# Optimization experiments

Measured on AMD Instinct MI355X. Metric: run time of the kernel, lower is better.

Reference implementation:

```python
import jax, jax.numpy as jnp
import numpy as np

B, S, D, H, L, K = 16, 384, 512, 8, 4, 7
HD = D // H
MAXLEN = 400


def _pos_encoding(d=D, max_len=MAXLEN):
    # Faithful to the (unusual) torch loop: even idx i -> sin(pos/10000**(2i/d)),
    # odd idx i+1 -> cos(pos/10000**(2(i+1)/d))
    pe = np.zeros((max_len, d), dtype=np.float32)
    pos = np.arange(max_len, dtype=np.float64)[:, None]
    i = np.arange(0, d, 2)
    pe[:, i] = np.sin(pos / 10000.0 ** (2 * i / d))
    pe[:, i + 1] = np.cos(pos / 10000.0 ** (2 * (i + 1) / d))
    return jnp.asarray(pe)

POS_ENC = _pos_encoding()


def layer_norm(x, g, b, eps=1e-5):
    m = jnp.mean(x, -1, keepdims=True)
    v = jnp.mean((x - m) ** 2, -1, keepdims=True)
    return (x - m) * jax.lax.rsqrt(v + eps) * g + b


def dsconv(x, dw_w, pw_w, pw_b):
    # x: [B,S,D]; depthwise conv1d (no bias) then pointwise 1x1 (bias)
    xc = jnp.transpose(x, (0, 2, 1))  # [B,D,S]
    y = jax.lax.conv_general_dilated(
        xc, dw_w, window_strides=(1,), padding=[(K // 2, K // 2)],
        dimension_numbers=("NCH", "OIH", "NCH"), feature_group_count=D)  # [B,D,S]
    return jnp.einsum("bcs,oc->bso", y, pw_w) + pw_b  # [B,S,D]


def setup_inputs():
    key = jax.random.key(0)
    ks = jax.random.split(key, 16)
    sc = 0.02
    inp = {
        "x": jax.random.normal(ks[0], (B, S, D), jnp.float32),
        "mask": jax.random.randint(ks[1], (B, S), 0, 2, jnp.int32),
        "dw_w": jax.random.normal(ks[2], (L, D, 1, K), jnp.float32) * sc,
        "pw_w": jax.random.normal(ks[3], (L, D, D), jnp.float32) * sc,
        "pw_b": jnp.zeros((L, D), jnp.float32),
        "conv_ln_g": jnp.ones((L, D), jnp.float32),
        "conv_ln_b": jnp.zeros((L, D), jnp.float32),
        "pos_ln_g": jnp.ones((D,), jnp.float32),
        "pos_ln_b": jnp.zeros((D,), jnp.float32),
        "wq": jax.random.normal(ks[4], (D, D), jnp.float32) * sc,
        "bq": jnp.zeros((D,), jnp.float32),
        "wk": jax.random.normal(ks[5], (D, D), jnp.float32) * sc,
        "bk": jnp.zeros((D,), jnp.float32),
        "wv": jax.random.normal(ks[6], (D, D), jnp.float32) * sc,
        "bv": jnp.zeros((D,), jnp.float32),
        "wo": jax.random.normal(ks[7], (D, D), jnp.float32) * sc,
        "bo": jnp.zeros((D,), jnp.float32),
        "ff_ln_g": jnp.ones((D,), jnp.float32),
        "ff_ln_b": jnp.zeros((D,), jnp.float32),
        "ff_w": jax.random.normal(ks[8], (D, D), jnp.float32) * sc,
        "ff_b": jnp.zeros((D,), jnp.float32),
    }
    return inp


def attention(x, mask, wq, bq, wk, bk, wv, bv, wo, bo):
    def heads(w, b):
        y = jnp.einsum("bsd,od->bso", x, w) + b
        return jnp.transpose(y.reshape(B, S, H, HD), (0, 2, 1, 3))  # [B,H,S,HD]
    q, k, v = heads(wq, bq), heads(wk, bk), heads(wv, bv)
    energy = jnp.einsum("bhqd,bhkd->bhqk", q, k) / jnp.sqrt(jnp.float32(HD))
    m = (mask == 1)[:, None, None, :]  # [B,1,1,S]
    energy = jnp.where(m, jnp.float32(-1e10), energy)
    alpha = jax.nn.softmax(energy, axis=-1)  # dropout = identity (eval)
    a = jnp.einsum("bhqk,bhkd->bhqd", alpha, v)
    a = jnp.transpose(a, (0, 2, 1, 3)).reshape(B, S, D)
    return jnp.einsum("bsd,od->bso", a, wo) + bo


def reference(x, mask, dw_w, pw_w, pw_b, conv_ln_g, conv_ln_b, pos_ln_g, pos_ln_b,
              wq, bq, wk, bk, wv, bv, wo, bo, ff_ln_g, ff_ln_b, ff_w, ff_b):
    out = x + POS_ENC[None, :S, :]
    res = out
    out = layer_norm(out, pos_ln_g, pos_ln_b)
    for i in range(L):
        out = jax.nn.relu(dsconv(out, dw_w[i], pw_w[i], pw_b[i]))
        out = out + res  # dropout = identity (eval)
        res = out
        out = layer_norm(out, conv_ln_g[i], conv_ln_b[i])
    out = attention(out, mask, wq, bq, wk, bk, wv, bv, wo, bo)
    out = out + res
    res = out
    out = layer_norm(out, ff_ln_g, ff_ln_b)
    out = jax.nn.relu(jnp.einsum("bsd,od->bso", out, ff_w) + ff_b)
    return out + res
```

## Files before the change

kernel.cpp:

```cpp
#include <hip/hip_runtime.h>

#define BB 16
#define SS 384
#define DD 512
#define HH 8
#define HDIM 64
#define LLAY 4
#define KW 7
#define MM (BB*SS)

typedef unsigned short u16;
typedef unsigned int u32;
typedef short short8v __attribute__((ext_vector_type(8)));
typedef float floatx4 __attribute__((ext_vector_type(4)));

__device__ __forceinline__ float bf2f(u16 u) {
    union { u32 i; float f; } v; v.i = ((u32)u) << 16; return v.f;
}
__device__ __forceinline__ u16 f2bf(float f) {
    union { float f; u32 i; } v; v.f = f;
    return (u16)((v.i + 0x7FFFu + ((v.i >> 16) & 1u)) >> 16);
}
__device__ __forceinline__ bool sniff_f32(const void* dtp) {
    return *((const u32*)dtp) == 0x3F800000u;
}
__device__ __forceinline__ float ldf(const void* p, long i, bool f32) {
    return f32 ? ((const float*)p)[i] : bf2f(((const u16*)p)[i]);
}
__device__ __forceinline__ short8v ldfrag_scalar(const void* p, long i, bool f32) {
    short8v r;
    if (f32) {
        const float* q = (const float*)p + i;
#pragma unroll
        for (int j = 0; j < 8; j++) r[j] = (short)f2bf(q[j]);
    } else {
        r = *(const short8v*)((const u16*)p + i);
    }
    return r;
}

__device__ __forceinline__ void load_lds16(const u16* g, u16* l) {
    __builtin_amdgcn_global_load_lds((const __attribute__((address_space(1))) void*)g,
                                     (__attribute__((address_space(3))) void*)l, 16, 0, 0);
}
__device__ __forceinline__ int swz(int row) { return (row & 3) ^ ((row >> 2) & 3); }
__device__ __forceinline__ short8v lds_frag(const u16* buf, int row, int quad) {
    return *(const short8v*)(buf + ((size_t)row * 4 + (quad ^ swz(row))) * 8);
}

#define WCV_DW 2359296
#define WCV_TOT (WCV_DW + LLAY*KW*DD)
__global__ __launch_bounds__(256) void cvt_weights_kernel(
    const void* __restrict__ pw_w, const void* __restrict__ wq,
    const void* __restrict__ wk, const void* __restrict__ wv,
    const void* __restrict__ wo, const void* __restrict__ ff_w,
    const void* __restrict__ dw_w,
    u16* __restrict__ dst, const void* __restrict__ dtp) {
    const bool f32 = sniff_f32(dtp);
    const int i = blockIdx.x * 256 + threadIdx.x;
    if (i >= WCV_TOT) return;
    const void* src; long idx;
    if (i < 1048576) { src = pw_w; idx = i; }
    else if (i < WCV_DW) {
        const int j = i - 1048576;
        const int m = j >> 18;
        idx = j & 262143;
        src = (m == 0) ? wq : (m == 1) ? wk : (m == 2) ? wv : (m == 3) ? wo : ff_w;
    } else {
        const int j = i - WCV_DW;
        const int l = j / (KW * DD);
        const int r1 = j % (KW * DD);
        const int t = r1 / DD, c = r1 % DD;
        src = dw_w; idx = ((long)l * DD + c) * KW + t;
    }
    dst[i] = f2bf(ldf(src, idx, f32));
}

__global__ __launch_bounds__(256) void posln_kernel(const void* __restrict__ x,
                                                    const void* __restrict__ g,
                                                    const void* __restrict__ bvec,
                                                    u16* __restrict__ res,
                                                    u16* __restrict__ out,
                                                    const void* __restrict__ dtp) {
    const bool f32 = sniff_f32(dtp);
    const int row = blockIdx.x;
    const int s = row % SS;
    const int tid = threadIdx.x;
    float v[2];
#pragma unroll
    for (int i = 0; i < 2; i++) {
        const int d = tid + i * 256;
        const float freq = __expf(-(float)d * 0.035977892078032f);
        const float arg = (float)s * freq;
        const float pe = (d & 1) ? cosf(arg) : sinf(arg);
        v[i] = ldf(x, (long)row * DD + d, f32) + pe;
        res[row * DD + d] = f2bf(v[i]);
    }
    float sum = v[0] + v[1], sq = v[0] * v[0] + v[1] * v[1];
#pragma unroll
    for (int off = 32; off; off >>= 1) { sum += __shfl_down(sum, off); sq += __shfl_down(sq, off); }
    __shared__ float red[4][2];
    const int wv = tid >> 6;
    if ((tid & 63) == 0) { red[wv][0] = sum; red[wv][1] = sq; }
    __syncthreads();
    sum = red[0][0] + red[1][0] + red[2][0] + red[3][0];
    sq  = red[0][1] + red[1][1] + red[2][1] + red[3][1];
    const float mean = sum * (1.f / DD);
    const float rstd = rsqrtf(sq * (1.f / DD) - mean * mean + 1e-5f);
#pragma unroll
    for (int i = 0; i < 2; i++) {
        const int d = tid + i * 256;
        out[row * DD + d] = f2bf((v[i] - mean) * rstd * ldf(g, d, f32) + ldf(bvec, d, f32));
    }
}

template <int VEC>
__global__ __launch_bounds__(256) void dwconv_kernel(const u16* __restrict__ in,
                                                     const void* __restrict__ w, int layer,
                                                     u16* __restrict__ out,
                                                     const void* __restrict__ dtp) {
    if constexpr (VEC) {
        const int bsw = (blockIdx.x & 7) * (MM * DD / 8 / 256 / 8) + (blockIdx.x >> 3);
        const int idx = bsw * 256 + threadIdx.x;
        const int c8 = (idx & 63) * 8;
        const int ms = idx >> 6;
        const int s = ms % SS;
        const u16* wl = (const u16*)w + (size_t)layer * KW * DD;
        float acc[8] = {0, 0, 0, 0, 0, 0, 0, 0};
#pragma unroll
        for (int t = 0; t < KW; t++) {
            const int ss2 = s + t - 3;
            if (ss2 >= 0 && ss2 < SS) {
                const short8v iv = *(const short8v*)(in + (size_t)(ms + t - 3) * DD + c8);
                const short8v wv = *(const short8v*)(wl + t * DD + c8);
#pragma unroll
                for (int j = 0; j < 8; j++)
                    acc[j] += bf2f((u16)iv[j]) * bf2f((u16)wv[j]);
            }
        }
        short8v ov;
#pragma unroll
        for (int j = 0; j < 8; j++) ov[j] = (short)f2bf(acc[j]);
        *(short8v*)(out + (size_t)ms * DD + c8) = ov;
    } else {
        const bool f32 = sniff_f32(dtp);
        const long woff = (long)layer * DD * KW;
        const int idx = blockIdx.x * 256 + threadIdx.x;
        const int c = idx & (DD - 1);
        const int ms = idx >> 9;
        const int s = ms % SS;
        float acc = 0.f;
#pragma unroll
        for (int t = 0; t < KW; t++) {
            const int ss2 = s + t - 3;
            if (ss2 >= 0 && ss2 < SS)
                acc += bf2f(in[(ms + t - 3) * DD + c]) * ldf(w, woff + c * KW + t, f32);
        }
        out[idx] = f2bf(acc);
    }
}

__device__ __forceinline__ void stage_tile(const u16* A, const u16* W, int m0,
                                           u16* Abuf, u16* Wbuf, int tid, int k0) {
#pragma unroll
    for (int j = 0; j < 8; j++) {
        const int c = j * 256 + tid;
        const int row = c >> 2;
        const int kpart = (c & 3) ^ swz(row);
        load_lds16(W + (size_t)row * DD + k0 + kpart * 8, Wbuf + (size_t)c * 8);
    }
    if (tid < 128) {
        const int row = tid >> 2;
        const int kpart = (tid & 3) ^ swz(row);
        load_lds16(A + (size_t)(m0 + row) * DD + k0 + kpart * 8, Abuf + (size_t)tid * 8);
    }
}

__device__ __forceinline__ void kloop_lds(const u16* A, const u16* W, int m0,
                                          u16* Abuf, u16* Wbuf,
                                          int tid, int wave, int ln15, int quad,
                                          floatx4 acc[2][8]) {
    stage_tile(A, W, m0, Abuf, Wbuf, tid, 0);
    __syncthreads();
    for (int ks = 0; ks < 16; ks++) {
        const int cur = ks & 1;
        u16* Ab = Abuf + cur * (32 * 32);
        u16* Wb = Wbuf + cur * (DD * 32);
        if (ks < 15)
            stage_tile(A, W, m0, Abuf + (cur ^ 1) * (32 * 32),
                       Wbuf + (cur ^ 1) * (DD * 32), tid, (ks + 1) * 32);
        const short8v a0 = lds_frag(Ab, ln15, quad);
        const short8v a1 = lds_frag(Ab, 16 + ln15, quad);
#pragma unroll
        for (int nt = 0; nt < 8; nt++) {
            const short8v b = lds_frag(Wb, wave * 128 + nt * 16 + ln15, quad);
            acc[0][nt] = __builtin_amdgcn_mfma_f32_16x16x32_bf16(a0, b, acc[0][nt], 0, 0, 0);
            acc[1][nt] = __builtin_amdgcn_mfma_f32_16x16x32_bf16(a1, b, acc[1][nt], 0, 0, 0);
        }
        __syncthreads();
    }
}

template <int RELU, int DO_LN, int FINAL, int WVEC>
__global__ __launch_bounds__(256, 2) void gemm32_kernel(
    const u16* __restrict__ A, const void* __restrict__ W, int wlayer,
    const void* __restrict__ bias, const void* __restrict__ g,
    const void* __restrict__ bvec, int blayer,
    const u16* __restrict__ res_in, u16* __restrict__ res_out,
    void* __restrict__ out, const void* __restrict__ dtp) {
    const bool f32 = sniff_f32(dtp);
    const long woff = (long)wlayer * DD * DD;
    const long voff = (long)blayer * DD;
    __shared__ float part[4][2][16][2];
    __shared__ __align__(16) u16 Wbuf[2 * DD * 32];
    __shared__ __align__(16) u16 Abuf[2 * 32 * 32];
    const int tid = threadIdx.x;
    const int m0 = blockIdx.x * 32;
    const int wave = tid >> 6, lane = tid & 63;
    const int ln15 = lane & 15, quad = lane >> 4;

    floatx4 acc[2][8];
#pragma unroll
    for (int mt = 0; mt < 2; mt++)
#pragma unroll
        for (int nt = 0; nt < 8; nt++) acc[mt][nt] = {0.f, 0.f, 0.f, 0.f};

    if constexpr (WVEC) {
        kloop_lds(A, (const u16*)W + woff, m0, Abuf, Wbuf, tid, wave, ln15, quad, acc);
    } else {
        const u16* A0 = A + (size_t)(m0 + ln15) * DD + quad * 8;
        const u16* A1 = A0 + 16 * DD;
#pragma unroll
        for (int ks = 0; ks < 16; ks++) {
            const int k0 = ks * 32;
            short8v a0 = *(const short8v*)(A0 + k0);
            short8v a1 = *(const short8v*)(A1 + k0);
            short8v b[8];
#pragma unroll
            for (int nt = 0; nt < 8; nt++) {
                const long wrow = woff + (long)(wave * 128 + nt * 16 + ln15) * DD + quad * 8 + k0;
                b[nt] = ldfrag_scalar(W, wrow, f32);
            }
#pragma unroll
            for (int nt = 0; nt < 8; nt++) {
                acc[0][nt] = __builtin_amdgcn_mfma_f32_16x16x32_bf16(a0, b[nt], acc[0][nt], 0, 0, 0);
                acc[1][nt] = __builtin_amdgcn_mfma_f32_16x16x32_bf16(a1, b[nt], acc[1][nt], 0, 0, 0);
            }
        }
    }

#pragma unroll
    for (int nt = 0; nt < 8; nt++) {
        const int col = wave * 128 + nt * 16 + ln15;
        const float bval = ldf(bias, voff + col, f32);
#pragma unroll
        for (int mt = 0; mt < 2; mt++)
#pragma unroll
            for (int r = 0; r < 4; r++) {
                const int m = m0 + mt * 16 + quad * 4 + r;
                float y = acc[mt][nt][r] + bval;
                if (RELU) y = fmaxf(y, 0.f);
                y += bf2f(res_in[(size_t)m * DD + col]);
                if (res_out) res_out[(size_t)m * DD + col] = f2bf(y);
                acc[mt][nt][r] = y;
            }
    }
    if constexpr (DO_LN) {
        float ls[2][4], lq[2][4];
#pragma unroll
        for (int mt = 0; mt < 2; mt++)
#pragma unroll
            for (int r = 0; r < 4; r++) {
                float s = 0.f, q = 0.f;
#pragma unroll
                for (int nt = 0; nt < 8; nt++) { const float y = acc[mt][nt][r]; s += y; q += y * y; }
                ls[mt][r] = s; lq[mt][r] = q;
            }
#pragma unroll
        for (int off = 1; off < 16; off <<= 1)
#pragma unroll
            for (int mt = 0; mt < 2; mt++)
#pragma unroll
                for (int r = 0; r < 4; r++) {
                    ls[mt][r] += __shfl_xor(ls[mt][r], off);
                    lq[mt][r] += __shfl_xor(lq[mt][r], off);
                }
        if (ln15 == 0) {
#pragma unroll
            for (int mt = 0; mt < 2; mt++)
#pragma unroll
                for (int r = 0; r < 4; r++) {
                    part[wave][mt][quad * 4 + r][0] = ls[mt][r];
                    part[wave][mt][quad * 4 + r][1] = lq[mt][r];
                }
        }
        __syncthreads();
        float mean[2][4], rstd[2][4];
#pragma unroll
        for (int mt = 0; mt < 2; mt++)
#pragma unroll
            for (int r = 0; r < 4; r++) {
                const int rr = quad * 4 + r;
                const float s = part[0][mt][rr][0] + part[1][mt][rr][0] + part[2][mt][rr][0] + part[3][mt][rr][0];
                const float q = part[0][mt][rr][1] + part[1][mt][rr][1] + part[2][mt][rr][1] + part[3][mt][rr][1];
                const float mn = s * (1.f / DD);
                mean[mt][r] = mn;
                rstd[mt][r] = rsqrtf(q * (1.f / DD) - mn * mn + 1e-5f);
            }
#pragma unroll
        for (int nt = 0; nt < 8; nt++) {
            const int col = wave * 128 + nt * 16 + ln15;
            const float gv = ldf(g, voff + col, f32);
            const float bv = ldf(bvec, voff + col, f32);
#pragma unroll
            for (int mt = 0; mt < 2; mt++)
#pragma unroll
                for (int r = 0; r < 4; r++) {
                    const int m = m0 + mt * 16 + quad * 4 + r;
                    ((u16*)out)[(size_t)m * DD + col] =
                        f2bf((acc[mt][nt][r] - mean[mt][r]) * rstd[mt][r] * gv + bv);
                }
        }
    } else {
#pragma unroll
        for (int nt = 0; nt < 8; nt++) {
            const int col = wave * 128 + nt * 16 + ln15;
#pragma unroll
            for (int mt = 0; mt < 2; mt++)
#pragma unroll
                for (int r = 0; r < 4; r++) {
                    const int m = m0 + mt * 16 + quad * 4 + r;
                    if (FINAL && f32) ((float*)out)[(size_t)m * DD + col] = acc[mt][nt][r];
                    else              ((u16*)out)[(size_t)m * DD + col] = f2bf(acc[mt][nt][r]);
                }
        }
    }
}

#define VPAD 40
template <int WVEC>
__global__ __launch_bounds__(256, 2) void qkv32_kernel(
    const u16* __restrict__ A,
    const void* __restrict__ Wq, const void* __restrict__ Wk, const void* __restrict__ Wv,
    const void* __restrict__ bq, const void* __restrict__ bk, const void* __restrict__ bv,
    u16* __restrict__ qo, u16* __restrict__ ko, u16* __restrict__ vo,
    const void* __restrict__ dtp) {
    const bool f32 = sniff_f32(dtp);
    const int sel = blockIdx.y;
    const void* W = (sel == 0) ? Wq : (sel == 1) ? Wk : Wv;
    const void* bias = (sel == 0) ? bq : (sel == 1) ? bk : bv;
    u16* out = (sel == 0) ? qo : (sel == 1) ? ko : vo;

    __shared__ __align__(16) u16 Wbuf[2 * DD * 32];
    __shared__ __align__(16) u16 Abuf[2 * 32 * 32];
    u16 (*vtile)[128][VPAD] = (u16 (*)[128][VPAD])Wbuf;

    const int tid = threadIdx.x;
    const int m0 = blockIdx.x * 32;
    const int wave = tid >> 6, lane = tid & 63;
    const int ln15 = lane & 15, quad = lane >> 4;
    const int bidx = m0 / SS;

    floatx4 acc[2][8];
#pragma unroll
    for (int mt = 0; mt < 2; mt++)
#pragma unroll
        for (int nt = 0; nt < 8; nt++) acc[mt][nt] = {0.f, 0.f, 0.f, 0.f};

    if constexpr (WVEC) {
        kloop_lds(A, (const u16*)W, m0, Abuf, Wbuf, tid, wave, ln15, quad, acc);
    } else {
        const u16* A0 = A + (size_t)(m0 + ln15) * DD + quad * 8;
        const u16* A1 = A0 + 16 * DD;
#pragma unroll
        for (int ks = 0; ks < 16; ks++) {
            const int k0 = ks * 32;
            short8v a0 = *(const short8v*)(A0 + k0);
            short8v a1 = *(const short8v*)(A1 + k0);
            short8v b[8];
#pragma unroll
            for (int nt = 0; nt < 8; nt++) {
                const long wrow = (long)(wave * 128 + nt * 16 + ln15) * DD + quad * 8 + k0;
                b[nt] = ldfrag_scalar(W, wrow, f32);
            }
#pragma unroll
            for (int nt = 0; nt < 8; nt++) {
                acc[0][nt] = __builtin_amdgcn_mfma_f32_16x16x32_bf16(a0, b[nt], acc[0][nt], 0, 0, 0);
                acc[1][nt] = __builtin_amdgcn_mfma_f32_16x16x32_bf16(a1, b[nt], acc[1][nt], 0, 0, 0);
            }
        }
    }

    if (sel == 2) {
#pragma unroll
        for (int nt = 0; nt < 8; nt++) {
            const int c = nt * 16 + ln15;
            const float bval = ldf(bias, wave * 128 + c, f32);
#pragma unroll
            for (int mt = 0; mt < 2; mt++)
#pragma unroll
                for (int r = 0; r < 4; r++)
                    vtile[wave][c][mt * 16 + quad * 4 + r] = f2bf(acc[mt][nt][r] + bval);
        }
        __builtin_amdgcn_s_waitcnt(0);
#pragma unroll
        for (int cc = 0; cc < 2; cc++) {
            const int c = lane * 2 + cc;
            const int col = wave * 128 + c;
            const int h = col >> 6, hd = col & 63;
            u16* dst = vo + ((size_t)(bidx * HH + h) * HDIM + hd) * SS + (m0 - bidx * SS);
            const u16* srcl = &vtile[wave][c][0];
#pragma unroll
            for (int j = 0; j < 4; j++)
                *(short8v*)(dst + j * 8) = *(const short8v*)(srcl + j * 8);
        }
    } else {
#pragma unroll
        for (int nt = 0; nt < 8; nt++) {
            const int col = wave * 128 + nt * 16 + ln15;
            const int h = col >> 6, hd = col & 63;
            const float bval = ldf(bias, col, f32);
#pragma unroll
            for (int mt = 0; mt < 2; mt++)
#pragma unroll
                for (int r = 0; r < 4; r++) {
                    const int m = m0 + mt * 16 + quad * 4 + r;
                    const int s = m - bidx * SS;
                    out[((size_t)(bidx * HH + h) * SS + s) * HDIM + hd] = f2bf(acc[mt][nt][r] + bval);
                }
        }
    }
}

#define SSPF 388
#define SSPH 392
__global__ __launch_bounds__(256) void attn_kernel(const u16* __restrict__ q,
                                                   const u16* __restrict__ k,
                                                   const u16* __restrict__ vT,
                                                   const int* __restrict__ mask,
                                                   u16* __restrict__ out) {
    __shared__ float sc[16 * SSPF];
    __shared__ float rsum[16];
    u16* al = (u16*)sc;

    const int n = blockIdx.x;
    const int i = n >> 3;
    const int g = (n & 7) * 16 + i / 24;
    const int qt = i % 24;
    const int h = g & 7, b = g >> 3;
    const int q0 = qt * 16;
    const int wave = threadIdx.x >> 6, lane = threadIdx.x & 63;
    const int ln15 = lane & 15, quad = lane >> 4;

    const u16* qh = q + (size_t)(b * HH + h) * SS * HDIM;
    const u16* kh = k + (size_t)(b * HH + h) * SS * HDIM;

    const short8v* arow = (const short8v*)(qh + (q0 + ln15) * HDIM + quad * 8);
    const short8v a0 = arow[0], a1 = arow[4];
#pragma unroll
    for (int t = 0; t < 6; t++) {
        const int n0 = wave * 96 + t * 16;
        const short8v* brow = (const short8v*)(kh + (n0 + ln15) * HDIM + quad * 8);
        floatx4 acc = {0.f, 0.f, 0.f, 0.f};
        __builtin_amdgcn_s_setprio(1);
        acc = __builtin_amdgcn_mfma_f32_16x16x32_bf16(a0, brow[0], acc, 0, 0, 0);
        acc = __builtin_amdgcn_mfma_f32_16x16x32_bf16(a1, brow[4], acc, 0, 0, 0);
        __builtin_amdgcn_s_setprio(0);
        const int kk = n0 + ln15;
        const bool msk = (mask[b * SS + kk] == 1);
#pragma unroll
        for (int r = 0; r < 4; r++) {
            float v = acc[r] * 0.125f;
            if (msk) v = -1e10f;
            sc[(quad * 4 + r) * SSPF + kk] = v;
        }
    }
    __syncthreads();
    const int r = threadIdx.x >> 4, cg = threadIdx.x & 15;
    float pv[24], mx = -3.0e38f;
#pragma unroll
    for (int j = 0; j < 24; j++) { pv[j] = sc[r * SSPF + cg + 16 * j]; mx = fmaxf(mx, pv[j]); }
#pragma unroll
    for (int off = 8; off; off >>= 1) mx = fmaxf(mx, __shfl_xor(mx, off, 16));
    float sum = 0.f;
#pragma unroll
    for (int j = 0; j < 24; j++) { const float p = __expf(pv[j] - mx); pv[j] = p; sum += p; }
#pragma unroll
    for (int off = 8; off; off >>= 1) sum += __shfl_xor(sum, off, 16);
    if (cg == 0) rsum[r] = sum;
    __syncthreads();
#pragma unroll
    for (int j = 0; j < 24; j++) al[r * SSPH + cg + 16 * j] = f2bf(pv[j]);
    __syncthreads();
    const u16* vh = vT + (size_t)(b * HH + h) * HDIM * SS;
    const int d0 = wave * 16;
    floatx4 acc = {0.f, 0.f, 0.f, 0.f};
    __builtin_amdgcn_s_setprio(1);
#pragma unroll
    for (int k0 = 0; k0 < SS; k0 += 32) {
        const short8v af = *(const short8v*)(al + ln15 * SSPH + k0 + quad * 8);
        const short8v bf = *(const short8v*)(vh + (d0 + ln15) * SS + k0 + quad * 8);
        acc = __builtin_amdgcn_mfma_f32_16x16x32_bf16(af, bf, acc, 0, 0, 0);
    }
    __builtin_amdgcn_s_setprio(0);
#pragma unroll
    for (int rr = 0; rr < 4; rr++) {
        const int lr = quad * 4 + rr;
        const int s = q0 + lr;
        out[((size_t)(b * SS + s)) * DD + h * HDIM + d0 + ln15] = f2bf(acc[rr] / rsum[lr]);
    }
}

extern "C" void kernel_launch(void* const* d_in, const int* in_sizes, int n_in,
                              void* d_out, int out_size, void* d_ws, size_t ws_size,
                              hipStream_t stream) {
    (void)in_sizes; (void)n_in; (void)out_size;
    const void* x     = d_in[0];
    const int*  mask  = (const int*)d_in[1];
    const void* dw_w  = d_in[2];
    const void* pw_w  = d_in[3];
    const void* pw_b  = d_in[4];
    const void* cln_g = d_in[5];
    const void* cln_b = d_in[6];
    const void* pln_g = d_in[7];
    const void* pln_b = d_in[8];
    const void* wq    = d_in[9];
    const void* bq    = d_in[10];
    const void* wk    = d_in[11];
    const void* bk    = d_in[12];
    const void* wv    = d_in[13];
    const void* bv    = d_in[14];
    const void* wo    = d_in[15];
    const void* bo    = d_in[16];
    const void* fln_g = d_in[17];
    const void* fln_b = d_in[18];
    const void* ff_w  = d_in[19];
    const void* ff_b  = d_in[20];
    const void* dtp   = cln_g;

    const size_t nAct = (size_t)MM * DD;
    char* p = (char*)d_ws;
    u16* res   = (u16*)p; p += nAct * 2;
    u16* lnout = (u16*)p; p += nAct * 2;
    u16* tmp   = (u16*)p; p += nAct * 2;
    u16* vT    = (u16*)p; p += nAct * 2;
    u16* wcv   = (u16*)p;
    u16* kb    = (u16*)d_out;

    const size_t needFast = nAct * 2 * 4 + (size_t)WCV_TOT * 2;
    const bool fast = (ws_size >= needFast);

    posln_kernel<<<MM, 256, 0, stream>>>(x, pln_g, pln_b, res, lnout, dtp);

    if (fast) {
        cvt_weights_kernel<<<(WCV_TOT + 255) / 256, 256, 0, stream>>>(
            pw_w, wq, wk, wv, wo, ff_w, dw_w, wcv, dtp);
        const u16* w_pw = wcv;
        const u16* w_q  = wcv + 1048576;
        const u16* w_k  = wcv + 1310720;
        const u16* w_v  = wcv + 1572864;
        const u16* w_o  = wcv + 1835008;
        const u16* w_ff = wcv + 2097152;
        const u16* w_dw = wcv + WCV_DW;

        for (int i = 0; i < LLAY; i++) {
            dwconv_kernel<1><<<MM * DD / 8 / 256, 256, 0, stream>>>(lnout, w_dw, i, tmp, dtp);
            gemm32_kernel<1, 1, 0, 1><<<MM / 32, 256, 0, stream>>>(
                tmp, w_pw + (size_t)i * DD * DD, 0, pw_b, cln_g, cln_b, i,
                res, res, lnout, dtp);
        }
        qkv32_kernel<1><<<dim3(MM / 32, 3), 256, 0, stream>>>(
            lnout, w_q, w_k, w_v, bq, bk, bv, tmp, kb, vT, dtp);

        attn_kernel<<<BB * HH * (SS / 16), 256, 0, stream>>>(tmp, kb, vT, mask, lnout);

        gemm32_kernel<0, 1, 0, 1><<<MM / 32, 256, 0, stream>>>(
            lnout, w_o, 0, bo, fln_g, fln_b, 0, res, res, lnout, dtp);
        gemm32_kernel<1, 0, 1, 1><<<MM / 32, 256, 0, stream>>>(
            lnout, w_ff, 0, ff_b, nullptr, nullptr, 0, res, nullptr, d_out, dtp);
    } else {
        for (int i = 0; i < LLAY; i++) {
            dwconv_kernel<0><<<MM * DD / 256, 256, 0, stream>>>(lnout, dw_w, i, tmp, dtp);
            gemm32_kernel<1, 1, 0, 0><<<MM / 32, 256, 0, stream>>>(
                tmp, pw_w, i, pw_b, cln_g, cln_b, i, res, res, lnout, dtp);
        }
        qkv32_kernel<0><<<dim3(MM / 32, 3), 256, 0, stream>>>(
            lnout, wq, wk, wv, bq, bk, bv, tmp, kb, vT, dtp);

        attn_kernel<<<BB * HH * (SS / 16), 256, 0, stream>>>(tmp, kb, vT, mask, lnout);

        gemm32_kernel<0, 1, 0, 0><<<MM / 32, 256, 0, stream>>>(
            lnout, wo, 0, bo, fln_g, fln_b, 0, res, res, lnout, dtp);
        gemm32_kernel<1, 0, 1, 0><<<MM / 32, 256, 0, stream>>>(
            lnout, ff_w, 0, ff_b, nullptr, nullptr, 0, res, nullptr, d_out, dtp);
    }
}
```

Measured before the change: 384.4 us.

## Shrink GEMM row tile to 16 with 512-thread blocks and merge posln with weight conversion

The row-panel GEMMs and the QKV projection now use a 16-row M tile with 8 waves, each covering 64 output columns, instead of 32 rows with 4 waves. This doubles the number of blocks to fill more CUs, at the cost of staging each full-width weight tile into LDS twice as often across the grid. The position-encoding/LayerNorm kernel and the weight-conversion kernel are merged into one launch, and sin/cos switch to fast intrinsics. The V-transpose epilogue and the LN reduction across waves are adapted to the new tile shape.

```diff
diff --git a/kernel.cpp b/kernel.cpp
--- a/kernel.cpp
+++ b/kernel.cpp
@@ -50,49 +50,47 @@
 
 #define WCV_DW 2359296
 #define WCV_TOT (WCV_DW + LLAY*KW*DD)
-__global__ __launch_bounds__(256) void cvt_weights_kernel(
+#define NCVB ((WCV_TOT + 255) / 256)
+
+__global__ __launch_bounds__(256) void posln_cvt_kernel(
+    const void* __restrict__ x, const void* __restrict__ g, const void* __restrict__ bvec,
+    u16* __restrict__ res, u16* __restrict__ out,
     const void* __restrict__ pw_w, const void* __restrict__ wq,
     const void* __restrict__ wk, const void* __restrict__ wv,
     const void* __restrict__ wo, const void* __restrict__ ff_w,
-    const void* __restrict__ dw_w,
-    u16* __restrict__ dst, const void* __restrict__ dtp) {
+    const void* __restrict__ dw_w, u16* __restrict__ wdst,
+    const void* __restrict__ dtp) {
     const bool f32 = sniff_f32(dtp);
-    const int i = blockIdx.x * 256 + threadIdx.x;
-    if (i >= WCV_TOT) return;
-    const void* src; long idx;
-    if (i < 1048576) { src = pw_w; idx = i; }
-    else if (i < WCV_DW) {
-        const int j = i - 1048576;
-        const int m = j >> 18;
-        idx = j & 262143;
-        src = (m == 0) ? wq : (m == 1) ? wk : (m == 2) ? wv : (m == 3) ? wo : ff_w;
-    } else {
-        const int j = i - WCV_DW;
-        const int l = j / (KW * DD);
-        const int r1 = j % (KW * DD);
-        const int t = r1 / DD, c = r1 % DD;
-        src = dw_w; idx = ((long)l * DD + c) * KW + t;
-    }
-    dst[i] = f2bf(ldf(src, idx, f32));
-}
-
-__global__ __launch_bounds__(256) void posln_kernel(const void* __restrict__ x,
-                                                    const void* __restrict__ g,
-                                                    const void* __restrict__ bvec,
-                                                    u16* __restrict__ res,
-                                                    u16* __restrict__ out,
-                                                    const void* __restrict__ dtp) {
-    const bool f32 = sniff_f32(dtp);
+    const int tid = threadIdx.x;
+    if (blockIdx.x >= MM) {
+        const int i = (blockIdx.x - MM) * 256 + tid;
+        if (i >= WCV_TOT) return;
+        const void* src; long idx;
+        if (i < 1048576) { src = pw_w; idx = i; }
+        else if (i < WCV_DW) {
+            const int j = i - 1048576;
+            const int m = j >> 18;
+            idx = j & 262143;
+            src = (m == 0) ? wq : (m == 1) ? wk : (m == 2) ? wv : (m == 3) ? wo : ff_w;
+        } else {
+            const int j = i - WCV_DW;
+            const int l = j / (KW * DD);
+            const int r1 = j % (KW * DD);
+            const int t = r1 / DD, c = r1 % DD;
+            src = dw_w; idx = ((long)l * DD + c) * KW + t;
+        }
+        wdst[i] = f2bf(ldf(src, idx, f32));
+        return;
+    }
     const int row = blockIdx.x;
     const int s = row % SS;
-    const int tid = threadIdx.x;
     float v[2];
 #pragma unroll
     for (int i = 0; i < 2; i++) {
         const int d = tid + i * 256;
         const float freq = __expf(-(float)d * 0.035977892078032f);
         const float arg = (float)s * freq;
-        const float pe = (d & 1) ? cosf(arg) : sinf(arg);
+        const float pe = (d & 1) ? __cosf(arg) : __sinf(arg);
         v[i] = ldf(x, (long)row * DD + d, f32) + pe;
         res[row * DD + d] = f2bf(v[i]);
     }
@@ -100,8 +98,8 @@
 #pragma unroll
     for (int off = 32; off; off >>= 1) { sum += __shfl_down(sum, off); sq += __shfl_down(sq, off); }
     __shared__ float red[4][2];
-    const int wv = tid >> 6;
-    if ((tid & 63) == 0) { red[wv][0] = sum; red[wv][1] = sq; }
+    const int wv2 = tid >> 6;
+    if ((tid & 63) == 0) { red[wv2][0] = sum; red[wv2][1] = sq; }
     __syncthreads();
     sum = red[0][0] + red[1][0] + red[2][0] + red[3][0];
     sq  = red[0][1] + red[1][1] + red[2][1] + red[3][1];
@@ -160,49 +158,47 @@
     }
 }
 
-__device__ __forceinline__ void stage_tile(const u16* A, const u16* W, int m0,
-                                           u16* Abuf, u16* Wbuf, int tid, int k0) {
-#pragma unroll
-    for (int j = 0; j < 8; j++) {
-        const int c = j * 256 + tid;
+__device__ __forceinline__ void stage_tile16(const u16* A, const u16* W, int m0,
+                                             u16* Abuf, u16* Wbuf, int tid, int k0) {
+#pragma unroll
+    for (int j = 0; j < 4; j++) {
+        const int c = j * 512 + tid;
         const int row = c >> 2;
         const int kpart = (c & 3) ^ swz(row);
         load_lds16(W + (size_t)row * DD + k0 + kpart * 8, Wbuf + (size_t)c * 8);
     }
-    if (tid < 128) {
+    if (tid < 64) {
         const int row = tid >> 2;
         const int kpart = (tid & 3) ^ swz(row);
         load_lds16(A + (size_t)(m0 + row) * DD + k0 + kpart * 8, Abuf + (size_t)tid * 8);
     }
 }
 
-__device__ __forceinline__ void kloop_lds(const u16* A, const u16* W, int m0,
-                                          u16* Abuf, u16* Wbuf,
-                                          int tid, int wave, int ln15, int quad,
-                                          floatx4 acc[2][8]) {
-    stage_tile(A, W, m0, Abuf, Wbuf, tid, 0);
+__device__ __forceinline__ void kloop16(const u16* A, const u16* W, int m0,
+                                        u16* Abuf, u16* Wbuf,
+                                        int tid, int wave, int ln15, int quad,
+                                        floatx4 acc[4]) {
+    stage_tile16(A, W, m0, Abuf, Wbuf, tid, 0);
     __syncthreads();
     for (int ks = 0; ks < 16; ks++) {
         const int cur = ks & 1;
-        u16* Ab = Abuf + cur * (32 * 32);
+        u16* Ab = Abuf + cur * (16 * 32);
         u16* Wb = Wbuf + cur * (DD * 32);
         if (ks < 15)
-            stage_tile(A, W, m0, Abuf + (cur ^ 1) * (32 * 32),
-                       Wbuf + (cur ^ 1) * (DD * 32), tid, (ks + 1) * 32);
+            stage_tile16(A, W, m0, Abuf + (cur ^ 1) * (16 * 32),
+                         Wbuf + (cur ^ 1) * (DD * 32), tid, (ks + 1) * 32);
         const short8v a0 = lds_frag(Ab, ln15, quad);
-        const short8v a1 = lds_frag(Ab, 16 + ln15, quad);
-#pragma unroll
-        for (int nt = 0; nt < 8; nt++) {
-            const short8v b = lds_frag(Wb, wave * 128 + nt * 16 + ln15, quad);
-            acc[0][nt] = __builtin_amdgcn_mfma_f32_16x16x32_bf16(a0, b, acc[0][nt], 0, 0, 0);
-            acc[1][nt] = __builtin_amdgcn_mfma_f32_16x16x32_bf16(a1, b, acc[1][nt], 0, 0, 0);
+#pragma unroll
+        for (int nt = 0; nt < 4; nt++) {
+            const short8v b = lds_frag(Wb, wave * 64 + nt * 16 + ln15, quad);
+            acc[nt] = __builtin_amdgcn_mfma_f32_16x16x32_bf16(a0, b, acc[nt], 0, 0, 0);
         }
         __syncthreads();
     }
 }
 
 template <int RELU, int DO_LN, int FINAL, int WVEC>
-__global__ __launch_bounds__(256, 2) void gemm32_kernel(
+__global__ __launch_bounds__(512, 4) void gemm16_kernel(
     const u16* __restrict__ A, const void* __restrict__ W, int wlayer,
     const void* __restrict__ bias, const void* __restrict__ g,
     const void* __restrict__ bvec, int blayer,
@@ -211,135 +207,116 @@
     const bool f32 = sniff_f32(dtp);
     const long woff = (long)wlayer * DD * DD;
     const long voff = (long)blayer * DD;
-    __shared__ float part[4][2][16][2];
+    __shared__ float part[8][16][2];
     __shared__ __align__(16) u16 Wbuf[2 * DD * 32];
-    __shared__ __align__(16) u16 Abuf[2 * 32 * 32];
+    __shared__ __align__(16) u16 Abuf[2 * 16 * 32];
     const int tid = threadIdx.x;
-    const int m0 = blockIdx.x * 32;
+    const int m0 = blockIdx.x * 16;
     const int wave = tid >> 6, lane = tid & 63;
     const int ln15 = lane & 15, quad = lane >> 4;
 
-    floatx4 acc[2][8];
-#pragma unroll
-    for (int mt = 0; mt < 2; mt++)
-#pragma unroll
-        for (int nt = 0; nt < 8; nt++) acc[mt][nt] = {0.f, 0.f, 0.f, 0.f};
+    floatx4 acc[4];
+#pragma unroll
+    for (int nt = 0; nt < 4; nt++) acc[nt] = {0.f, 0.f, 0.f, 0.f};
 
     if constexpr (WVEC) {
-        kloop_lds(A, (const u16*)W + woff, m0, Abuf, Wbuf, tid, wave, ln15, quad, acc);
+        kloop16(A, (const u16*)W + woff, m0, Abuf, Wbuf, tid, wave, ln15, quad, acc);
     } else {
         const u16* A0 = A + (size_t)(m0 + ln15) * DD + quad * 8;
-        const u16* A1 = A0 + 16 * DD;
 #pragma unroll
         for (int ks = 0; ks < 16; ks++) {
             const int k0 = ks * 32;
             short8v a0 = *(const short8v*)(A0 + k0);
-            short8v a1 = *(const short8v*)(A1 + k0);
-            short8v b[8];
-#pragma unroll
-            for (int nt = 0; nt < 8; nt++) {
-                const long wrow = woff + (long)(wave * 128 + nt * 16 + ln15) * DD + quad * 8 + k0;
+            short8v b[4];
+#pragma unroll
+            for (int nt = 0; nt < 4; nt++) {
+                const long wrow = woff + (long)(wave * 64 + nt * 16 + ln15) * DD + quad * 8 + k0;
                 b[nt] = ldfrag_scalar(W, wrow, f32);
             }
 #pragma unroll
-            for (int nt = 0; nt < 8; nt++) {
-                acc[0][nt] = __builtin_amdgcn_mfma_f32_16x16x32_bf16(a0, b[nt], acc[0][nt], 0, 0, 0);
-                acc[1][nt] = __builtin_amdgcn_mfma_f32_16x16x32_bf16(a1, b[nt], acc[1][nt], 0, 0, 0);
-            }
-        }
-    }
-
-#pragma unroll
-    for (int nt = 0; nt < 8; nt++) {
-        const int col = wave * 128 + nt * 16 + ln15;
+            for (int nt = 0; nt < 4; nt++)
+                acc[nt] = __builtin_amdgcn_mfma_f32_16x16x32_bf16(a0, b[nt], acc[nt], 0, 0, 0);
+        }
+    }
+
+#pragma unroll
+    for (int nt = 0; nt < 4; nt++) {
+        const int col = wave * 64 + nt * 16 + ln15;
         const float bval = ldf(bias, voff + col, f32);
 #pragma unroll
-        for (int mt = 0; mt < 2; mt++)
+        for (int r = 0; r < 4; r++) {
+            const int m = m0 + quad * 4 + r;
+            float y = acc[nt][r] + bval;
+            if (RELU) y = fmaxf(y, 0.f);
+            y += bf2f(res_in[(size_t)m * DD + col]);
+            if (res_out) res_out[(size_t)m * DD + col] = f2bf(y);
+            acc[nt][r] = y;
+        }
+    }
+    if constexpr (DO_LN) {
+        float ls[4], lq[4];
+#pragma unroll
+        for (int r = 0; r < 4; r++) {
+            float s = 0.f, q = 0.f;
+#pragma unroll
+            for (int nt = 0; nt < 4; nt++) { const float y = acc[nt][r]; s += y; q += y * y; }
+            ls[r] = s; lq[r] = q;
+        }
+#pragma unroll
+        for (int off = 1; off < 16; off <<= 1)
 #pragma unroll
             for (int r = 0; r < 4; r++) {
-                const int m = m0 + mt * 16 + quad * 4 + r;
-                float y = acc[mt][nt][r] + bval;
-                if (RELU) y = fmaxf(y, 0.f);
-                y += bf2f(res_in[(size_t)m * DD + col]);
-                if (res_out) res_out[(size_t)m * DD + col] = f2bf(y);
-                acc[mt][nt][r] = y;
-            }
-    }
-    if constexpr (DO_LN) {
-        float ls[2][4], lq[2][4];
-#pragma unroll
-        for (int mt = 0; mt < 2; mt++)
+                ls[r] += __shfl_xor(ls[r], off);
+                lq[r] += __shfl_xor(lq[r], off);
+            }
+        if (ln15 == 0) {
 #pragma unroll
             for (int r = 0; r < 4; r++) {
-                float s = 0.f, q = 0.f;
-#pragma unroll
-                for (int nt = 0; nt < 8; nt++) { const float y = acc[mt][nt][r]; s += y; q += y * y; }
-                ls[mt][r] = s; lq[mt][r] = q;
-            }
-#pragma unroll
-        for (int off = 1; off < 16; off <<= 1)
-#pragma unroll
-            for (int mt = 0; mt < 2; mt++)
-#pragma unroll
-                for (int r = 0; r < 4; r++) {
-                    ls[mt][r] += __shfl_xor(ls[mt][r], off);
-                    lq[mt][r] += __shfl_xor(lq[mt][r], off);
-                }
-        if (ln15 == 0) {
-#pragma unroll
-            for (int mt = 0; mt < 2; mt++)
-#pragma unroll
-                for (int r = 0; r < 4; r++) {
-                    part[wave][mt][quad * 4 + r][0] = ls[mt][r];
-                    part[wave][mt][quad * 4 + r][1] = lq[mt][r];
-                }
+                part[wave][quad * 4 + r][0] = ls[r];
+                part[wave][quad * 4 + r][1] = lq[r];
+            }
         }
         __syncthreads();
-        float mean[2][4], rstd[2][4];
-#pragma unroll
-        for (int mt = 0; mt < 2; mt++)
-#pragma unroll
-            for (int r = 0; r < 4; r++) {
-                const int rr = quad * 4 + r;
-                const float s = part[0][mt][rr][0] + part[1][mt][rr][0] + part[2][mt][rr][0] + part[3][mt][rr][0];
-                const float q = part[0][mt][rr][1] + part[1][mt][rr][1] + part[2][mt][rr][1] + part[3][mt][rr][1];
-                const float mn = s * (1.f / DD);
-                mean[mt][r] = mn;
-                rstd[mt][r] = rsqrtf(q * (1.f / DD) - mn * mn + 1e-5f);
-            }
-#pragma unroll
-        for (int nt = 0; nt < 8; nt++) {
-            const int col = wave * 128 + nt * 16 + ln15;
+        float mean[4], rstd[4];
+#pragma unroll
+        for (int r = 0; r < 4; r++) {
+            const int rr = quad * 4 + r;
+            float s = 0.f, q = 0.f;
+#pragma unroll
+            for (int wv = 0; wv < 8; wv++) { s += part[wv][rr][0]; q += part[wv][rr][1]; }
+            const float mn = s * (1.f / DD);
+            mean[r] = mn;
+            rstd[r] = rsqrtf(q * (1.f / DD) - mn * mn + 1e-5f);
+        }
+#pragma unroll
+        for (int nt = 0; nt < 4; nt++) {
+            const int col = wave * 64 + nt * 16 + ln15;
             const float gv = ldf(g, voff + col, f32);
             const float bv = ldf(bvec, voff + col, f32);
 #pragma unroll
-            for (int mt = 0; mt < 2; mt++)
-#pragma unroll
-                for (int r = 0; r < 4; r++) {
-                    const int m = m0 + mt * 16 + quad * 4 + r;
-                    ((u16*)out)[(size_t)m * DD + col] =
-                        f2bf((acc[mt][nt][r] - mean[mt][r]) * rstd[mt][r] * gv + bv);
-                }
-        }
-    } else {
-#pragma unroll
-        for (int nt = 0; nt < 8; nt++) {
-            const int col = wave * 128 + nt * 16 + ln15;
-#pragma unroll
-            for (int mt = 0; mt < 2; mt++)
-#pragma unroll
-                for (int r = 0; r < 4; r++) {
-                    const int m = m0 + mt * 16 + quad * 4 + r;
-                    if (FINAL && f32) ((float*)out)[(size_t)m * DD + col] = acc[mt][nt][r];
-                    else              ((u16*)out)[(size_t)m * DD + col] = f2bf(acc[mt][nt][r]);
-                }
+            for (int r = 0; r < 4; r++) {
+                const int m = m0 + quad * 4 + r;
+                ((u16*)out)[(size_t)m * DD + col] =
+                    f2bf((acc[nt][r] - mean[r]) * rstd[r] * gv + bv);
+            }
+        }
+    } else {
+#pragma unroll
+        for (int nt = 0; nt < 4; nt++) {
+            const int col = wave * 64 + nt * 16 + ln15;
+#pragma unroll
+            for (int r = 0; r < 4; r++) {
+                const int m = m0 + quad * 4 + r;
+                if (FINAL && f32) ((float*)out)[(size_t)m * DD + col] = acc[nt][r];
+                else              ((u16*)out)[(size_t)m * DD + col] = f2bf(acc[nt][r]);
+            }
         }
     }
 }
 
 #define VPAD 40
 template <int WVEC>
-__global__ __launch_bounds__(256, 2) void qkv32_kernel(
+__global__ __launch_bounds__(512, 4) void qkv16_kernel(
     const u16* __restrict__ A,
     const void* __restrict__ Wq, const void* __restrict__ Wk, const void* __restrict__ Wv,
     const void* __restrict__ bq, const void* __restrict__ bk, const void* __restrict__ bv,
@@ -352,82 +329,71 @@
     u16* out = (sel == 0) ? qo : (sel == 1) ? ko : vo;
 
     __shared__ __align__(16) u16 Wbuf[2 * DD * 32];
-    __shared__ __align__(16) u16 Abuf[2 * 32 * 32];
-    u16 (*vtile)[128][VPAD] = (u16 (*)[128][VPAD])Wbuf;
+    __shared__ __align__(16) u16 Abuf[2 * 16 * 32];
+    u16 (*vtile)[64][VPAD] = (u16 (*)[64][VPAD])Wbuf;
 
     const int tid = threadIdx.x;
-    const int m0 = blockIdx.x * 32;
+    const int m0 = blockIdx.x * 16;
     const int wave = tid >> 6, lane = tid & 63;
     const int ln15 = lane & 15, quad = lane >> 4;
     const int bidx = m0 / SS;
 
-    floatx4 acc[2][8];
-#pragma unroll
-    for (int mt = 0; mt < 2; mt++)
-#pragma unroll
-        for (int nt = 0; nt < 8; nt++) acc[mt][nt] = {0.f, 0.f, 0.f, 0.f};
+    floatx4 acc[4];
+#pragma unroll
+    for (int nt = 0; nt < 4; nt++) acc[nt] = {0.f, 0.f, 0.f, 0.f};
 
     if constexpr (WVEC) {
-        kloop_lds(A, (const u16*)W, m0, Abuf, Wbuf, tid, wave, ln15, quad, acc);
+        kloop16(A, (const u16*)W, m0, Abuf, Wbuf, tid, wave, ln15, quad, acc);
     } else {
         const u16* A0 = A + (size_t)(m0 + ln15) * DD + quad * 8;
-        const u16* A1 = A0 + 16 * DD;
 #pragma unroll
         for (int ks = 0; ks < 16; ks++) {
             const int k0 = ks * 32;
             short8v a0 = *(const short8v*)(A0 + k0);
-            short8v a1 = *(const short8v*)(A1 + k0);
-            short8v b[8];
-#pragma unroll
-            for (int nt = 0; nt < 8; nt++) {
-                const long wrow = (long)(wave * 128 + nt * 16 + ln15) * DD + quad * 8 + k0;
+            short8v b[4];
+#pragma unroll
+            for (int nt = 0; nt < 4; nt++) {
+                const long wrow = (long)(wave * 64 + nt * 16 + ln15) * DD + quad * 8 + k0;
                 b[nt] = ldfrag_scalar(W, wrow, f32);
             }
 #pragma unroll
-            for (int nt = 0; nt < 8; nt++) {
-                acc[0][nt] = __builtin_amdgcn_mfma_f32_16x16x32_bf16(a0, b[nt], acc[0][nt], 0, 0, 0);
-                acc[1][nt] = __builtin_amdgcn_mfma_f32_16x16x32_bf16(a1, b[nt], acc[1][nt], 0, 0, 0);
-            }
+            for (int nt = 0; nt < 4; nt++)
+                acc[nt] = __builtin_amdgcn_mfma_f32_16x16x32_bf16(a0, b[nt], acc[nt], 0, 0, 0);
         }
     }
 
     if (sel == 2) {
 #pragma unroll
-        for (int nt = 0; nt < 8; nt++) {
+        for (int nt = 0; nt < 4; nt++) {
             const int c = nt * 16 + ln15;
-            const float bval = ldf(bias, wave * 128 + c, f32);
-#pragma unroll
-            for (int mt = 0; mt < 2; mt++)
-#pragma unroll
-                for (int r = 0; r < 4; r++)
-                    vtile[wave][c][mt * 16 + quad * 4 + r] = f2bf(acc[mt][nt][r] + bval);
+            const float bval = ldf(bias, wave * 64 + c, f32);
+#pragma unroll
+            for (int r = 0; r < 4; r++)
+                vtile[wave][c][quad * 4 + r] = f2bf(acc[nt][r] + bval);
         }
         __builtin_amdgcn_s_waitcnt(0);
-#pragma unroll
-        for (int cc = 0; cc < 2; cc++) {
-            const int c = lane * 2 + cc;
-            const int col = wave * 128 + c;
+        {
+            const int c = lane;
+            const int col = wave * 64 + c;
             const int h = col >> 6, hd = col & 63;
             u16* dst = vo + ((size_t)(bidx * HH + h) * HDIM + hd) * SS + (m0 - bidx * SS);
             const u16* srcl = &vtile[wave][c][0];
 #pragma unroll
-            for (int j = 0; j < 4; j++)
+            for (int j = 0; j < 2; j++)
                 *(short8v*)(dst + j * 8) = *(const short8v*)(srcl + j * 8);
         }
     } else {
 #pragma unroll
-        for (int nt = 0; nt < 8; nt++) {
-            const int col = wave * 128 + nt * 16 + ln15;
+        for (int nt = 0; nt < 4; nt++) {
+            const int col = wave * 64 + nt * 16 + ln15;
             const int h = col >> 6, hd = col & 63;
             const float bval = ldf(bias, col, f32);
 #pragma unroll
-            for (int mt = 0; mt < 2; mt++)
-#pragma unroll
-                for (int r = 0; r < 4; r++) {
-                    const int m = m0 + mt * 16 + quad * 4 + r;
-                    const int s = m - bidx * SS;
-                    out[((size_t)(bidx * HH + h) * SS + s) * HDIM + hd] = f2bf(acc[mt][nt][r] + bval);
-                }
+            for (int r = 0; r < 4; r++) {
+                const int m = m0 + quad * 4 + r;
+                const int s = m - bidx * SS;
+                out[((size_t)(bidx * HH + h) * SS + s) * HDIM + hd] = f2bf(acc[nt][r] + bval);
+            }
         }
     }
 }
@@ -550,10 +516,9 @@
     const size_t needFast = nAct * 2 * 4 + (size_t)WCV_TOT * 2;
     const bool fast = (ws_size >= needFast);
 
-    posln_kernel<<<MM, 256, 0, stream>>>(x, pln_g, pln_b, res, lnout, dtp);
-
     if (fast) {
-        cvt_weights_kernel<<<(WCV_TOT + 255) / 256, 256, 0, stream>>>(
+        posln_cvt_kernel<<<MM + NCVB, 256, 0, stream>>>(
+            x, pln_g, pln_b, res, lnout,
             pw_w, wq, wk, wv, wo, ff_w, dw_w, wcv, dtp);
         const u16* w_pw = wcv;
         const u16* w_q  = wcv + 1048576;
@@ -565,33 +530,36 @@
 
         for (int i = 0; i < LLAY; i++) {
             dwconv_kernel<1><<<MM * DD / 8 / 256, 256, 0, stream>>>(lnout, w_dw, i, tmp, dtp);
-            gemm32_kernel<1, 1, 0, 1><<<MM / 32, 256, 0, stream>>>(
+            gemm16_kernel<1, 1, 0, 1><<<MM / 16, 512, 0, stream>>>(
                 tmp, w_pw + (size_t)i * DD * DD, 0, pw_b, cln_g, cln_b, i,
                 res, res, lnout, dtp);
         }
-        qkv32_kernel<1><<<dim3(MM / 32, 3), 256, 0, stream>>>(
+        qkv16_kernel<1><<<dim3(MM / 16, 3), 512, 0, stream>>>(
             lnout, w_q, w_k, w_v, bq, bk, bv, tmp, kb, vT, dtp);
 
         attn_kernel<<<BB * HH * (SS / 16), 256, 0, stream>>>(tmp, kb, vT, mask, lnout);
 
-        gemm32_kernel<0, 1, 0, 1><<<MM / 32, 256, 0, stream>>>(
+        gemm16_kernel<0, 1, 0, 1><<<MM / 16, 512, 0, stream>>>(
             lnout, w_o, 0, bo, fln_g, fln_b, 0, res, res, lnout, dtp);
-        gemm32_kernel<1, 0, 1, 1><<<MM / 32, 256, 0, stream>>>(
+        gemm16_kernel<1, 0, 1, 1><<<MM / 16, 512, 0, stream>>>(
             lnout, w_ff, 0, ff_b, nullptr, nullptr, 0, res, nullptr, d_out, dtp);
     } else {
+        posln_cvt_kernel<<<MM, 256, 0, stream>>>(
+            x, pln_g, pln_b, res, lnout,
+            pw_w, wq, wk, wv, wo, ff_w, dw_w, (u16*)d_ws, dtp);
         for (int i = 0; i < LLAY; i++) {
             dwconv_kernel<0><<<MM * DD / 256, 256, 0, stream>>>(lnout, dw_w, i, tmp, dtp);
-            gemm32_kernel<1, 1, 0, 0><<<MM / 32, 256, 0, stream>>>(
+            gemm16_kernel<1, 1, 0, 0><<<MM / 16, 512, 0, stream>>>(
                 tmp, pw_w, i, pw_b, cln_g, cln_b, i, res, res, lnout, dtp);
         }
-        qkv32_kernel<0><<<dim3(MM / 32, 3), 256, 0, stream>>>(
+        qkv16_kernel<0><<<dim3(MM / 16, 3), 512, 0, stream>>>(
             lnout, wq, wk, wv, bq, bk, bv, tmp, kb, vT, dtp);
 
         attn_kernel<<<BB * HH * (SS / 16), 256, 0, stream>>>(tmp, kb, vT, mask, lnout);
 
-        gemm32_kernel<0, 1, 0, 0><<<MM / 32, 256, 0, stream>>>(
+        gemm16_kernel<0, 1, 0, 0><<<MM / 16, 512, 0, stream>>>(
             lnout, wo, 0, bo, fln_g, fln_b, 0, res, res, lnout, dtp);
-        gemm32_kernel<1, 0, 1, 0><<<MM / 32, 256, 0, stream>>>(
+        gemm16_kernel<1, 0, 1, 0><<<MM / 16, 512, 0, stream>>>(
             lnout, ff_w, 0, ff_b, nullptr, nullptr, 0, res, nullptr, d_out, dtp);
     }
 }
```

Result: faster. 367.4 us (-4.4%).
